# Kernel tuning notes

Measured on AMD Instinct MI355X. Metric: run time of the kernel, lower is better.

Reference implementation:

```python
import jax, jax.numpy as jnp
import numpy as np

N_NODES = 50000


def gcn_conv(x, W, b, row, col, n):
    """PyG GCNConv with default add_self_loops=True, normalize=True.
    out[i] = sum_{e: col[e]=i} d^-1/2[row[e]] d^-1/2[i] * (x@W)[row[e]]
             + d^-1[i]*(x@W)[i] + b,  where d = in-degree + 1 (self-loop).
    """
    x_lin = x @ W                                   # [n, out_ch]
    ones = jnp.ones(row.shape[0], dtype=x.dtype)
    deg = jax.ops.segment_sum(ones, col, num_segments=n) + 1.0  # self-loop
    dinv = jax.lax.rsqrt(deg)                       # deg >= 1, safe
    norm = dinv[row] * dinv[col]                    # [E]
    msg = norm[:, None] * x_lin[row]                # [E, out_ch]
    agg = jax.ops.segment_sum(msg, col, num_segments=n)
    self_term = (dinv * dinv)[:, None] * x_lin      # self-loop contribution
    return agg + self_term + b


def setup_inputs() -> dict:
    key = jax.random.key(0)
    ks = jax.random.split(key, 10)
    in_ch, hid, out_ch = 128, 256, 64
    E = 800000
    x = jax.random.normal(ks[0], (N_NODES, in_ch), dtype=jnp.float32)
    edge_attr = jax.random.normal(ks[1], (E, 8), dtype=jnp.float32)  # unused by forward
    edge_index = jax.random.randint(ks[2], (2, E), 0, N_NODES, dtype=jnp.int64)
    def glorot(k, fan_in, fan_out):
        s = float(np.sqrt(6.0 / (fan_in + fan_out)))
        return jax.random.uniform(k, (fan_in, fan_out), jnp.float32, -s, s)
    return {
        "x": x,
        "edge_attr": edge_attr,
        "edge_index": edge_index,
        "W1": glorot(ks[3], in_ch, hid), "b1": jnp.zeros((hid,), jnp.float32),
        "W2": glorot(ks[4], hid, hid),  "b2": jnp.zeros((hid,), jnp.float32),
        "W3": glorot(ks[5], hid, out_ch), "b3": jnp.zeros((out_ch,), jnp.float32),
    }


def reference(x, edge_attr, edge_index, W1, b1, W2, b2, W3, b3):
    n = x.shape[0]
    row, col = edge_index[0], edge_index[1]
    h = jax.nn.sigmoid(gcn_conv(x, W1, b1, row, col, n))
    h = jax.nn.sigmoid(gcn_conv(h, W2, b2, row, col, n))
    # dropout(p=0.1) in eval mode is identity
    return gcn_conv(h, W3, b3, row, col, n)
```

## Files before the change

### kernel.cpp

```cpp
#include <hip/hip_runtime.h>
#include <hip/hip_bf16.h>

typedef __bf16 bf16x8_t __attribute__((ext_vector_type(8)));
typedef float f32x4_t __attribute__((ext_vector_type(4)));
typedef float f32x2_t __attribute__((ext_vector_type(2)));

__device__ __forceinline__ float bits2f(unsigned int u) {
    union { unsigned int u; float f; } c; c.u = u; return c.f;
}
__device__ __forceinline__ unsigned short f2bf_bits(float f) {
    __hip_bfloat16 h = __float2bfloat16(f);
    return __builtin_bit_cast(unsigned short, h);
}
__device__ __forceinline__ f32x2_t unpack_bf2(unsigned int u) {
    return (f32x2_t){bits2f(u << 16), bits2f(u & 0xffff0000u)};
}

__global__ void sentinel_fill(float* __restrict__ out, int n) {
    int i = blockIdx.x * blockDim.x + threadIdx.x;
    if (i < n) out[i] = 100.0f;
}

__global__ void detect_ei(const unsigned int* __restrict__ ei, int* __restrict__ flags) {
    int lane = threadIdx.x;
    int cz = 0;
    #pragma unroll
    for (int j = 0; j < 4; ++j) {
        int idx = lane * 4 + j;
        cz += (ei[2 * idx + 1] == 0u);
    }
    #pragma unroll
    for (int off = 32; off; off >>= 1) cz += __shfl_down(cz, off);
    if (lane == 0) flags[0] = (cz > 200);
}


__global__ void count_rank_dual2(const int* __restrict__ ei, int* __restrict__ cnt,
                                 int* __restrict__ rank, int* __restrict__ c32,
                                 int* __restrict__ r32, int E, int M,
                                 const int* __restrict__ flags) {
    int e = blockIdx.x * blockDim.x + threadIdx.x;
    if (e < E) {
        int r, c;
        if (flags[0]) { r = ei[2 * e]; c = ei[2 * E + 2 * e]; }
        else          { r = ei[e];     c = ei[E + e]; }
        c32[e] = c;
        r32[e] = r;
        int rk = 0;
        if ((unsigned)c < (unsigned)M) rk = atomicAdd(&cnt[c], 1);
        rank[e] = rk;
    }
}

__global__ void scan_blocks(const int* __restrict__ cnt, int* __restrict__ excl,
                            int* __restrict__ bsum, int n) {
    int tid = threadIdx.x;
    int i = blockIdx.x * 256 + tid;
    int lane = tid & 63, wv = tid >> 6;
    __shared__ int ws[4];
    int v = (i < n) ? cnt[i] : 0;
    int s = v;
    #pragma unroll
    for (int off = 1; off < 64; off <<= 1) {
        int t = __shfl_up(s, off);
        if (lane >= off) s += t;
    }
    if (lane == 63) ws[wv] = s;
    __syncthreads();
    if (tid == 0) { int a = 0; for (int q = 0; q < 4; ++q) { int t = ws[q]; ws[q] = a; a += t; } }
    __syncthreads();
    int ex = s - v + ws[wv];
    if (i < n) excl[i] = ex;
    if (tid == 255) bsum[blockIdx.x] = ex + v;
}

__global__ void scan_bsums(const int* __restrict__ bsum, int* __restrict__ boff,
                           int nb, int* __restrict__ colptr, int n) {
    int tid = threadIdx.x, lane = tid & 63, wv = tid >> 6;
    __shared__ int ws[4];
    __shared__ int carry;
    if (tid == 0) carry = 0;
    __syncthreads();
    for (int base = 0; base < nb; base += 256) {
        int i = base + tid;
        int v = (i < nb) ? bsum[i] : 0;
        int s = v;
        #pragma unroll
        for (int off = 1; off < 64; off <<= 1) {
            int t = __shfl_up(s, off);
            if (lane >= off) s += t;
        }
        if (lane == 63) ws[wv] = s;
        __syncthreads();
        if (tid == 0) { int a = carry; for (int q = 0; q < 4; ++q) { int t = ws[q]; ws[q] = a; a += t; } carry = a; }
        __syncthreads();
        int ex = s - v + ws[wv];
        if (i < nb) boff[i] = ex;
        __syncthreads();
    }
    if (tid == 0) colptr[n] = carry;
}

__global__ void scan_add_dinv(const int* __restrict__ excl, const int* __restrict__ boff,
                              const int* __restrict__ cnt, int* __restrict__ colptr,
                              float* __restrict__ dinv, int n) {
    int i = blockIdx.x * 256 + threadIdx.x;
    if (i < n) {
        colptr[i] = excl[i] + boff[blockIdx.x];
        dinv[i] = rsqrtf((float)cnt[i] + 1.0f);
    }
}

__global__ void fill_csr_part2(const int* __restrict__ c32, const int* __restrict__ r32,
                               const int* __restrict__ colptr, const int* __restrict__ rank,
                               int* __restrict__ esrc, int E, int M, int psz) {
    int part = blockIdx.x & 7;
    int e = (blockIdx.x >> 3) * 256 + threadIdx.x;
    int lo = part * psz;
    int hi = lo + psz; if (hi > M) hi = M;
    if (e < E) {
        int c = c32[e];
        if (c >= lo && c < hi) {
            int r = r32[e];
            if ((unsigned)r < (unsigned)M) {
                int p = colptr[c] + rank[e];
                if ((unsigned)p < (unsigned)E) esrc[p] = r;
            }
        }
    }
}

__global__ void prep_fused(const float* __restrict__ x, const float* __restrict__ dinv,
                           unsigned char* __restrict__ xs8,
                           const float* __restrict__ W1, const float* __restrict__ W2,
                           const float* __restrict__ W3,
                           unsigned short* __restrict__ Wt1, unsigned short* __restrict__ Wt2,
                           unsigned short* __restrict__ Wt3,
                           int M, int nps) {
    if ((int)blockIdx.x < nps) {
        int i = blockIdx.x * 256 + threadIdx.x;
        if (i < M * 32) {
            int row = i >> 5;
            float dv = dinv[row];
            float4 v = *(const float4*)(x + (size_t)i * 4);
            unsigned u = __builtin_amdgcn_cvt_pk_fp8_f32(v.x * dv, v.y * dv, 0, false);
            u = __builtin_amdgcn_cvt_pk_fp8_f32(v.z * dv, v.w * dv, u, true);
            *(unsigned*)(xs8 + (size_t)i * 4) = u;
        }
    } else {
        int i = ((int)blockIdx.x - nps) * 256 + threadIdx.x;
        if (i < 32768) {
            int k = i >> 8, n = i & 255;
            Wt1[n * 128 + k] = f2bf_bits(W1[i]);
        } else if (i < 32768 + 65536) {
            int j = i - 32768;
            int k = j >> 8, n = j & 255;
            Wt2[n * 256 + k] = f2bf_bits(W2[j]);
        } else if (i < 114688) {
            int j = i - 98304;
            int k = j >> 6, n = j & 63;
            Wt3[n * 256 + k] = f2bf_bits(W3[j]);
        }
    }
}

template<int K, int BN, int NTOT, int EPI>
__global__ __launch_bounds__(256) void gemm_tile(
    const __bf16* __restrict__ A,
    const unsigned short* __restrict__ Bt,
    const float* __restrict__ dinv,
    const float* __restrict__ bias,
    void* __restrict__ Y,
    int M)
{
    constexpr int KS = (K > 128) ? 128 : K;
    constexpr int KP = KS + 8;
    constexpr int NT = BN / 2 / 16;
    __shared__ unsigned short Bs[BN * KP];

    const int tid  = threadIdx.x;
    const int lane = tid & 63;
    const int wave = tid >> 6;
    const int wm   = wave >> 1;
    const int wn   = wave & 1;
    const int quad = lane >> 4;
    const int l16  = lane & 15;
    const int n0   = blockIdx.y * BN;

    int mrow[4];
#pragma unroll
    for (int mt = 0; mt < 4; ++mt) {
        int r = blockIdx.x * 128 + wm * 64 + mt * 16 + l16;
        mrow[mt] = (r < M) ? r : (M - 1);
    }

    f32x4_t acc[4][NT];
#pragma unroll
    for (int mt = 0; mt < 4; ++mt)
#pragma unroll
        for (int t = 0; t < NT; ++t) acc[mt][t] = (f32x4_t){0.f, 0.f, 0.f, 0.f};

    const unsigned short* BsW = &Bs[(wn * (BN / 2)) * KP];

    for (int kh = 0; kh < K; kh += KS) {
        constexpr int CH = BN * KS / 8;
        for (int idx = tid; idx < CH; idx += 256) {
            int n  = idx / (KS / 8);
            int k8 = idx - n * (KS / 8);
            uint4 v = *(const uint4*)(Bt + (size_t)(n0 + n) * K + kh + k8 * 8);
            *(uint4*)&Bs[n * KP + k8 * 8] = v;
        }
        __syncthreads();

#pragma unroll
        for (int kc = 0; kc < KS; kc += 32) {
            bf16x8_t a[4], b[NT];
#pragma unroll
            for (int mt = 0; mt < 4; ++mt)
                a[mt] = *(const bf16x8_t*)(A + (size_t)mrow[mt] * K + kh + kc + quad * 8);
#pragma unroll
            for (int t = 0; t < NT; ++t)
                b[t] = *(const bf16x8_t*)&BsW[(t * 16 + l16) * KP + kc + quad * 8];
#pragma unroll
            for (int mt = 0; mt < 4; ++mt)
#pragma unroll
                for (int t = 0; t < NT; ++t)
                    acc[mt][t] = __builtin_amdgcn_mfma_f32_16x16x32_bf16(a[mt], b[t], acc[mt][t], 0, 0, 0);
        }
        if (kh + KS < K) __syncthreads();
    }

    float bv[NT];
    if constexpr (EPI == 1) {
#pragma unroll
        for (int t = 0; t < NT; ++t)
            bv[t] = bias[n0 + wn * (BN / 2) + t * 16 + l16];
    }

#pragma unroll
    for (int mt = 0; mt < 4; ++mt) {
        int rowbase = blockIdx.x * 128 + wm * 64 + mt * 16 + quad * 4;
#pragma unroll
        for (int r = 0; r < 4; ++r) {
            int rrow = rowbase + r;
            if (rrow < M) {
                if constexpr (EPI == 0) {
                    float dv = dinv[rrow];
#pragma unroll
                    for (int t = 0; t < NT; ++t) {
                        int ccol = n0 + wn * (BN / 2) + t * 16 + l16;
                        ((__hip_bfloat16*)Y)[(size_t)rrow * NTOT + ccol] =
                            __float2bfloat16(acc[mt][t][r] * dv);
                    }
                } else if constexpr (EPI == 1) {
#pragma unroll
                    for (int t = 0; t < NT; ++t) {
                        int ccol = n0 + wn * (BN / 2) + t * 16 + l16;
                        float o = acc[mt][t][r] + bv[t];
                        o = 1.f / (1.f + __expf(-o));
                        ((__hip_bfloat16*)Y)[(size_t)rrow * NTOT + ccol] = __float2bfloat16(o);
                    }
                } else {
                    float dv = dinv[rrow];
#pragma unroll
                    for (int t = 0; t < NT; ++t) {
                        int ccol = n0 + wn * (BN / 2) + t * 16 + l16;
                        float o = acc[mt][t][r] * dv;
                        int pk = __builtin_amdgcn_cvt_pk_fp8_f32(o, o, 0, false);
                        ((unsigned char*)Y)[(size_t)rrow * NTOT + ccol] = (unsigned char)(pk & 0xff);
                    }
                }
            }
        }
    }
}

__global__ __launch_bounds__(256) void aggregate_fp8_v4(
    const unsigned char* __restrict__ Y8,
    const int* __restrict__ colptr,
    const int* __restrict__ esrc,
    const float* __restrict__ dinv,
    const float* __restrict__ bias,
    unsigned short* __restrict__ H,
    int M, int Etot)
{
    const int lane = threadIdx.x & 63;
    const int wave = threadIdx.x >> 6;
    int node = blockIdx.x * 4 + wave;
    if (node >= M) return;

    int s = colptr[node];
    int e = colptr[node + 1];
    if (s < 0) s = 0;
    if (e > Etot) e = Etot;
    if (e < s) e = s;
    int n = e - s;

    const char* Yb = (const char*)Y8;
    const unsigned lb = (unsigned)(lane * 4);

    unsigned su = *(const unsigned*)(Yb + (((unsigned)node) << 8) + lb);

    f32x2_t a0 = {0.f, 0.f}, a1 = {0.f, 0.f};

    auto gather8 = [&](unsigned* u, int base) {
        #pragma unroll
        for (int k = 0; k < 8; ++k) {
            unsigned off = (((unsigned)esrc[s + base + k]) << 8) + lb;
            u[k] = *(const unsigned*)(Yb + off);
        }
    };
    auto acc8 = [&](const unsigned* u) {
        #pragma unroll
        for (int k = 0; k < 8; ++k) {
            a0 += __builtin_amdgcn_cvt_pk_f32_fp8(u[k], false);
            a1 += __builtin_amdgcn_cvt_pk_f32_fp8(u[k], true);
        }
    };

    unsigned ua[8], ub[8];
    int NB = n >> 3;
    if (NB > 0) {
        gather8(ua, 0);
        int i = 1;
        for (; i + 1 < NB; i += 2) {
            gather8(ub, i << 3);
            acc8(ua);
            gather8(ua, (i + 1) << 3);
            acc8(ub);
        }
        if (i < NB) {
            gather8(ub, i << 3);
            acc8(ua);
            acc8(ub);
        } else {
            acc8(ua);
        }
    }
    #pragma unroll 2
    for (int t = NB << 3; t < n; ++t) {
        unsigned off = (((unsigned)esrc[s + t]) << 8) + lb;
        unsigned u = *(const unsigned*)(Yb + off);
        a0 += __builtin_amdgcn_cvt_pk_f32_fp8(u, false);
        a1 += __builtin_amdgcn_cvt_pk_f32_fp8(u, true);
    }
    a0 += __builtin_amdgcn_cvt_pk_f32_fp8(su, false);
    a1 += __builtin_amdgcn_cvt_pk_f32_fp8(su, true);

    float dv = dinv[node];
    float4 bv = *(const float4*)(bias + lane * 4);
    float o0 = a0[0] * dv + bv.x;
    float o1 = a0[1] * dv + bv.y;
    float o2 = a1[0] * dv + bv.z;
    float o3 = a1[1] * dv + bv.w;
    o0 = 1.f / (1.f + __expf(-o0));
    o1 = 1.f / (1.f + __expf(-o1));
    o2 = 1.f / (1.f + __expf(-o2));
    o3 = 1.f / (1.f + __expf(-o3));
    uint2 st;
    st.x = (unsigned)f2bf_bits(o0) | ((unsigned)f2bf_bits(o1) << 16);
    st.y = (unsigned)f2bf_bits(o2) | ((unsigned)f2bf_bits(o3) << 16);
    *(uint2*)(H + (size_t)node * 256 + lane * 4) = st;
}

__global__ __launch_bounds__(256) void aggregate_xs8(
    const unsigned char* __restrict__ X8,
    const int* __restrict__ colptr,
    const int* __restrict__ esrc,
    const float* __restrict__ dinv,
    unsigned short* __restrict__ xa,
    int M, int Etot)
{
    const int lane = threadIdx.x & 63;
    const int wave = threadIdx.x >> 6;
    const int l5 = lane & 31;
    const int g  = lane >> 5;
    int node = blockIdx.x * 4 + wave;
    if (node >= M) return;

    int s = colptr[node];
    int e = colptr[node + 1];
    if (s < 0) s = 0;
    if (e > Etot) e = Etot;
    if (e < s) e = s;
    int n = e - s;

    const char* Yb = (const char*)X8;
    const unsigned lb = (unsigned)(l5 * 4);

    unsigned su = 0;
    if (g == 0) su = *(const unsigned*)(Yb + (((unsigned)node) << 7) + lb);

    f32x2_t a0 = {0.f, 0.f}, a1 = {0.f, 0.f};

    auto gather4 = [&](unsigned* u, int base) {
        #pragma unroll
        for (int k = 0; k < 4; ++k) {
            unsigned off = (((unsigned)esrc[s + base + 2 * k + g]) << 7) + lb;
            u[k] = *(const unsigned*)(Yb + off);
        }
    };
    auto acc4 = [&](const unsigned* u) {
        #pragma unroll
        for (int k = 0; k < 4; ++k) {
            a0 += __builtin_amdgcn_cvt_pk_f32_fp8(u[k], false);
            a1 += __builtin_amdgcn_cvt_pk_f32_fp8(u[k], true);
        }
    };

    unsigned ua[4], ub[4];
    int NB = n >> 3;
    if (NB > 0) {
        gather4(ua, 0);
        int i = 1;
        for (; i + 1 < NB; i += 2) {
            gather4(ub, i << 3);
            acc4(ua);
            gather4(ua, (i + 1) << 3);
            acc4(ub);
        }
        if (i < NB) {
            gather4(ub, i << 3);
            acc4(ua);
            acc4(ub);
        } else {
            acc4(ua);
        }
    }
    for (int t = NB << 3; t + g < n; t += 2) {
        unsigned off = (((unsigned)esrc[s + t + g]) << 7) + lb;
        unsigned u = *(const unsigned*)(Yb + off);
        a0 += __builtin_amdgcn_cvt_pk_f32_fp8(u, false);
        a1 += __builtin_amdgcn_cvt_pk_f32_fp8(u, true);
    }
    if (g == 0) {
        a0 += __builtin_amdgcn_cvt_pk_f32_fp8(su, false);
        a1 += __builtin_amdgcn_cvt_pk_f32_fp8(su, true);
    }

    a0[0] += __shfl_xor(a0[0], 32);
    a0[1] += __shfl_xor(a0[1], 32);
    a1[0] += __shfl_xor(a1[0], 32);
    a1[1] += __shfl_xor(a1[1], 32);

    if (g == 0) {
        float dv = dinv[node];
        uint2 st;
        st.x = (unsigned)f2bf_bits(a0[0] * dv) | ((unsigned)f2bf_bits(a0[1] * dv) << 16);
        st.y = (unsigned)f2bf_bits(a1[0] * dv) | ((unsigned)f2bf_bits(a1[1] * dv) << 16);
        *(uint2*)(xa + (size_t)node * 128 + l5 * 4) = st;
    }
}

__global__ __launch_bounds__(256) void aggregate_bf16_64_v4(
    const unsigned short* __restrict__ Yin,
    const int* __restrict__ colptr,
    const int* __restrict__ esrc,
    const float* __restrict__ dinv,
    const float* __restrict__ bias,
    float* __restrict__ out,
    int M, int Etot)
{
    const int lane = threadIdx.x & 63;
    const int wave = threadIdx.x >> 6;
    const int l5 = lane & 31;
    const int g  = lane >> 5;
    int node = blockIdx.x * 4 + wave;
    if (node >= M) return;

    int s = colptr[node];
    int e = colptr[node + 1];
    if (s < 0) s = 0;
    if (e > Etot) e = Etot;
    if (e < s) e = s;
    int n = e - s;

    const char* Yb = (const char*)Yin;
    const unsigned lb = (unsigned)(l5 * 4);

    unsigned su = 0;
    if (g == 0) su = *(const unsigned*)(Yb + (((unsigned)node) << 7) + lb);

    f32x2_t a = {0.f, 0.f};

    auto gather4 = [&](unsigned* u, int base) {
        #pragma unroll
        for (int k = 0; k < 4; ++k) {
            unsigned off = (((unsigned)esrc[s + base + 2 * k + g]) << 7) + lb;
            u[k] = *(const unsigned*)(Yb + off);
        }
    };
    auto acc4 = [&](const unsigned* u) {
        #pragma unroll
        for (int k = 0; k < 4; ++k) a += unpack_bf2(u[k]);
    };

    unsigned ua[4], ub[4];
    int NB = n >> 3;
    if (NB > 0) {
        gather4(ua, 0);
        int i = 1;
        for (; i + 1 < NB; i += 2) {
            gather4(ub, i << 3);
            acc4(ua);
            gather4(ua, (i + 1) << 3);
            acc4(ub);
        }
        if (i < NB) {
            gather4(ub, i << 3);
            acc4(ua);
            acc4(ub);
        } else {
            acc4(ua);
        }
    }
    for (int t = NB << 3; t + g < n; t += 2) {
        unsigned off = (((unsigned)esrc[s + t + g]) << 7) + lb;
        unsigned u = *(const unsigned*)(Yb + off);
        a += unpack_bf2(u);
    }
    if (g == 0) a += unpack_bf2(su);

    a[0] += __shfl_xor(a[0], 32);
    a[1] += __shfl_xor(a[1], 32);

    if (g == 0) {
        float dv = dinv[node];
        float2 bv = *(const float2*)(bias + l5 * 2);
        float2 st;
        st.x = a[0] * dv + bv.x;
        st.y = a[1] * dv + bv.y;
        *(float2*)(out + (size_t)node * 64 + l5 * 2) = st;
    }
}


extern "C" void kernel_launch(void* const* d_in, const int* in_sizes, int n_in,
                              void* d_out, int out_size, void* d_ws, size_t ws_size,
                              hipStream_t stream)
{
    int iEI = 2, iW1 = 3, iB1 = 4, iW2 = 5, iB2 = 6, iW3 = 7, iB3 = 8;
    if (n_in == 8) { iEI = 1; iW1 = 2; iB1 = 3; iW2 = 4; iB2 = 5; iW3 = 6; iB3 = 7; }

    const float* x  = (const float*)d_in[0];
    const int* ei   = (const int*)d_in[iEI];
    const float* W1 = (const float*)d_in[iW1];
    const float* b1 = (const float*)d_in[iB1];
    const float* W2 = (const float*)d_in[iW2];
    const float* b2 = (const float*)d_in[iB2];
    const float* W3 = (const float*)d_in[iW3];
    const float* b3 = (const float*)d_in[iB3];

    const int M = in_sizes[0] / 128;
    const int E = in_sizes[iEI] / 2;
    const int NB = (M + 255) / 256;
    const int PSZ = (M + 7) / 8;

    auto rnd = [](size_t b) { return (b + 255) & ~(size_t)255; };
    size_t needed = rnd(64 * 4)
                  + rnd((size_t)M * 4) * 2
                  + rnd((size_t)(M + 1) * 4)
                  + rnd((size_t)M * 4)
                  + rnd((size_t)(NB + 1) * 4) * 2
                  + rnd((size_t)E * 4) * 4
                  + rnd((size_t)256 * 128 * 2)
                  + rnd((size_t)256 * 256 * 2)
                  + rnd((size_t)64 * 256 * 2)
                  + rnd((size_t)M * 256 * 2) * 2;
    if (ws_size < needed) {
        sentinel_fill<<<(out_size + 255) / 256, 256, 0, stream>>>((float*)d_out, out_size);
        return;
    }

    char* p = (char*)d_ws;
    auto alloc = [&](size_t bytes) {
        char* r = p;
        p += (bytes + 255) & ~(size_t)255;
        return r;
    };
    int* flags  = (int*)alloc(64 * 4);
    float* dinv = (float*)alloc((size_t)M * 4);
    int* cnt    = (int*)alloc((size_t)M * 4);
    int* colptr = (int*)alloc((size_t)(M + 1) * 4);
    int* excl   = (int*)alloc((size_t)M * 4);
    int* bsum   = (int*)alloc((size_t)(NB + 1) * 4);
    int* boff   = (int*)alloc((size_t)(NB + 1) * 4);
    int* esrc   = (int*)alloc((size_t)E * 4);
    int* rank   = (int*)alloc((size_t)E * 4);
    int* c32    = (int*)alloc((size_t)E * 4);
    int* r32    = (int*)alloc((size_t)E * 4);
    unsigned short* Wt1 = (unsigned short*)alloc((size_t)256 * 128 * 2);
    unsigned short* Wt2 = (unsigned short*)alloc((size_t)256 * 256 * 2);
    unsigned short* Wt3 = (unsigned short*)alloc((size_t)64 * 256 * 2);
    __hip_bfloat16* ybuf = (__hip_bfloat16*)alloc((size_t)M * 256 * 2);
    __hip_bfloat16* hbuf = (__hip_bfloat16*)alloc((size_t)M * 256 * 2);

    unsigned char* xs8 = (unsigned char*)ybuf;
    unsigned short* xa = (unsigned short*)ybuf + (size_t)M * 128;
    unsigned char*  y8 = (unsigned char*)ybuf;

    detect_ei<<<1, 64, 0, stream>>>((const unsigned int*)ei, flags);

    hipMemsetAsync(cnt, 0, (size_t)M * 4, stream);
    count_rank_dual2<<<(E + 255) / 256, 256, 0, stream>>>(ei, cnt, rank, c32, r32, E, M, flags);
    scan_blocks<<<NB, 256, 0, stream>>>(cnt, excl, bsum, M);
    scan_bsums<<<1, 256, 0, stream>>>(bsum, boff, NB, colptr, M);
    scan_add_dinv<<<NB, 256, 0, stream>>>(excl, boff, cnt, colptr, dinv, M);
    fill_csr_part2<<<((E + 255) / 256) * 8, 256, 0, stream>>>(
        c32, r32, colptr, rank, esrc, E, M, PSZ);

    int gmb = (M + 127) / 128;
    int ga  = (M + 3) / 4;
    int nps = (M * 32 + 255) / 256;

    prep_fused<<<nps + 448, 256, 0, stream>>>(
        x, dinv, xs8, W1, W2, W3, Wt1, Wt2, Wt3, M, nps);

    aggregate_xs8<<<ga, 256, 0, stream>>>(
        xs8, colptr, esrc, dinv, xa, M, E);
    gemm_tile<128, 128, 256, 1><<<dim3(gmb, 2), 256, 0, stream>>>(
        (const __bf16*)xa, Wt1, dinv, b1, hbuf, M);
    gemm_tile<256, 128, 256, 2><<<dim3(gmb, 2), 256, 0, stream>>>(
        (const __bf16*)hbuf, Wt2, dinv, b2, y8, M);
    aggregate_fp8_v4<<<ga, 256, 0, stream>>>(
        y8, colptr, esrc, dinv, b2, (unsigned short*)hbuf, M, E);
    gemm_tile<256, 64, 64, 0><<<dim3(gmb, 1), 256, 0, stream>>>(
        (const __bf16*)hbuf, Wt3, dinv, b3, ybuf, M);
    aggregate_bf16_64_v4<<<ga, 256, 0, stream>>>(
        (const unsigned short*)ybuf, colptr, esrc, dinv, b3, (float*)d_out, M, E);
}
```

Baseline: 329.6 us.

## Split fp8 layer-2 features into 128-column chunks and aggregate each chunk separately

The layer-2 GEMM epilogue now writes the fp8 output in two column-chunk planes of 128 bytes per row instead of 256-byte rows. The aggregation kernel is rewritten so each block handles one chunk for a group of nodes. Each wave splits its edges between two half-waves that each gather 128-byte rows, and the partial sums are combined with a cross-lane shuffle. The aim is to shrink the working set per chunk so gathered rows fit better in L2 and to interleave the chunk blocks of neighbouring node groups, at the cost of reading colptr/esrc twice and doing an extra reduction.

```diff
diff --git a/kernel.cpp b/kernel.cpp
--- a/kernel.cpp
+++ b/kernel.cpp
@@ -267,7 +267,9 @@
                         int ccol = n0 + wn * (BN / 2) + t * 16 + l16;
                         float o = acc[mt][t][r] * dv;
                         int pk = __builtin_amdgcn_cvt_pk_fp8_f32(o, o, 0, false);
-                        ((unsigned char*)Y)[(size_t)rrow * NTOT + ccol] = (unsigned char)(pk & 0xff);
+                        size_t choff = (size_t)(ccol >> 7) * ((size_t)M * 128)
+                                     + (size_t)rrow * 128 + (ccol & 127);
+                        ((unsigned char*)Y)[choff] = (unsigned char)(pk & 0xff);
                     }
                 }
             }
@@ -275,18 +277,25 @@
     }
 }
 
-__global__ __launch_bounds__(256) void aggregate_fp8_v4(
-    const unsigned char* __restrict__ Y8,
+__global__ __launch_bounds__(256) void aggregate_fp8_x2(
+    const unsigned char* __restrict__ Y8c,
     const int* __restrict__ colptr,
     const int* __restrict__ esrc,
     const float* __restrict__ dinv,
     const float* __restrict__ bias,
     unsigned short* __restrict__ H,
-    int M, int Etot)
+    int M, int Etot, int ga)
 {
     const int lane = threadIdx.x & 63;
     const int wave = threadIdx.x >> 6;
-    int node = blockIdx.x * 4 + wave;
+    const int l5 = lane & 31;
+    const int g2 = lane >> 5;
+
+    int s8 = blockIdx.x & 7;
+    int chunk = s8 >> 2;
+    int grp = (blockIdx.x >> 3) * 4 + (s8 & 3);
+    if (grp >= ga) return;
+    int node = grp * 4 + wave;
     if (node >= M) return;
 
     int s = colptr[node];
@@ -296,71 +305,81 @@
     if (e < s) e = s;
     int n = e - s;
 
-    const char* Yb = (const char*)Y8;
-    const unsigned lb = (unsigned)(lane * 4);
-
-    unsigned su = *(const unsigned*)(Yb + (((unsigned)node) << 8) + lb);
+    const char* Yb = (const char*)(Y8c + (size_t)chunk * ((size_t)M * 128));
+    const unsigned lb = (unsigned)(l5 * 4);
+
+    unsigned su = 0;
+    if (g2 == 0) su = *(const unsigned*)(Yb + ((unsigned)node) * 128u + lb);
 
     f32x2_t a0 = {0.f, 0.f}, a1 = {0.f, 0.f};
 
-    auto gather8 = [&](unsigned* u, int base) {
+    auto gather4 = [&](unsigned* u, int base) {
         #pragma unroll
-        for (int k = 0; k < 8; ++k) {
-            unsigned off = (((unsigned)esrc[s + base + k]) << 8) + lb;
+        for (int k = 0; k < 4; ++k) {
+            unsigned off = (((unsigned)esrc[s + base + 2 * k + g2]) * 128u) + lb;
             u[k] = *(const unsigned*)(Yb + off);
         }
     };
-    auto acc8 = [&](const unsigned* u) {
+    auto acc4 = [&](const unsigned* u) {
         #pragma unroll
-        for (int k = 0; k < 8; ++k) {
+        for (int k = 0; k < 4; ++k) {
             a0 += __builtin_amdgcn_cvt_pk_f32_fp8(u[k], false);
             a1 += __builtin_amdgcn_cvt_pk_f32_fp8(u[k], true);
         }
     };
 
-    unsigned ua[8], ub[8];
+    unsigned ua[4], ub[4];
     int NB = n >> 3;
     if (NB > 0) {
-        gather8(ua, 0);
+        gather4(ua, 0);
         int i = 1;
         for (; i + 1 < NB; i += 2) {
-            gather8(ub, i << 3);
-            acc8(ua);
-            gather8(ua, (i + 1) << 3);
-            acc8(ub);
+            gather4(ub, i << 3);
+            acc4(ua);
+            gather4(ua, (i + 1) << 3);
+            acc4(ub);
         }
         if (i < NB) {
-            gather8(ub, i << 3);
-            acc8(ua);
-            acc8(ub);
+            gather4(ub, i << 3);
+            acc4(ua);
+            acc4(ub);
         } else {
-            acc8(ua);
-        }
-    }
-    #pragma unroll 2
-    for (int t = NB << 3; t < n; ++t) {
-        unsigned off = (((unsigned)esrc[s + t]) << 8) + lb;
+            acc4(ua);
+        }
+    }
+    for (int t = NB << 3; t + g2 < n; t += 2) {
+        unsigned off = (((unsigned)esrc[s + t + g2]) * 128u) + lb;
         unsigned u = *(const unsigned*)(Yb + off);
         a0 += __builtin_amdgcn_cvt_pk_f32_fp8(u, false);
         a1 += __builtin_amdgcn_cvt_pk_f32_fp8(u, true);
     }
-    a0 += __builtin_amdgcn_cvt_pk_f32_fp8(su, false);
-    a1 += __builtin_amdgcn_cvt_pk_f32_fp8(su, true);
-
-    float dv = dinv[node];
-    float4 bv = *(const float4*)(bias + lane * 4);
-    float o0 = a0[0] * dv + bv.x;
-    float o1 = a0[1] * dv + bv.y;
-    float o2 = a1[0] * dv + bv.z;
-    float o3 = a1[1] * dv + bv.w;
-    o0 = 1.f / (1.f + __expf(-o0));
-    o1 = 1.f / (1.f + __expf(-o1));
-    o2 = 1.f / (1.f + __expf(-o2));
-    o3 = 1.f / (1.f + __expf(-o3));
-    uint2 st;
-    st.x = (unsigned)f2bf_bits(o0) | ((unsigned)f2bf_bits(o1) << 16);
-    st.y = (unsigned)f2bf_bits(o2) | ((unsigned)f2bf_bits(o3) << 16);
-    *(uint2*)(H + (size_t)node * 256 + lane * 4) = st;
+    if (g2 == 0) {
+        a0 += __builtin_amdgcn_cvt_pk_f32_fp8(su, false);
+        a1 += __builtin_amdgcn_cvt_pk_f32_fp8(su, true);
+    }
+
+    a0[0] += __shfl_xor(a0[0], 32);
+    a0[1] += __shfl_xor(a0[1], 32);
+    a1[0] += __shfl_xor(a1[0], 32);
+    a1[1] += __shfl_xor(a1[1], 32);
+
+    if (g2 == 0) {
+        float dv = dinv[node];
+        int chb = chunk * 128 + l5 * 4;
+        float4 bv = *(const float4*)(bias + chb);
+        float o0 = a0[0] * dv + bv.x;
+        float o1 = a0[1] * dv + bv.y;
+        float o2 = a1[0] * dv + bv.z;
+        float o3 = a1[1] * dv + bv.w;
+        o0 = 1.f / (1.f + __expf(-o0));
+        o1 = 1.f / (1.f + __expf(-o1));
+        o2 = 1.f / (1.f + __expf(-o2));
+        o3 = 1.f / (1.f + __expf(-o3));
+        uint2 st;
+        st.x = (unsigned)f2bf_bits(o0) | ((unsigned)f2bf_bits(o1) << 16);
+        st.y = (unsigned)f2bf_bits(o2) | ((unsigned)f2bf_bits(o3) << 16);
+        *(uint2*)(H + (size_t)node * 256 + chb) = st;
+    }
 }
 
 __global__ __launch_bounds__(256) void aggregate_xs8(
@@ -612,6 +631,7 @@
     int gmb = (M + 127) / 128;
     int ga  = (M + 3) / 4;
     int nps = (M * 32 + 255) / 256;
+    int nsup = (ga + 3) / 4;
 
     prep_fused<<<nps + 448, 256, 0, stream>>>(
         x, dinv, xs8, W1, W2, W3, Wt1, Wt2, Wt3, M, nps);
@@ -622,8 +642,8 @@
         (const __bf16*)xa, Wt1, dinv, b1, hbuf, M);
     gemm_tile<256, 128, 256, 2><<<dim3(gmb, 2), 256, 0, stream>>>(
         (const __bf16*)hbuf, Wt2, dinv, b2, y8, M);
-    aggregate_fp8_v4<<<ga, 256, 0, stream>>>(
-        y8, colptr, esrc, dinv, b2, (unsigned short*)hbuf, M, E);
+    aggregate_fp8_x2<<<nsup * 8, 256, 0, stream>>>(
+        y8, colptr, esrc, dinv, b2, (unsigned short*)hbuf, M, E, ga);
     gemm_tile<256, 64, 64, 0><<<dim3(gmb, 1), 256, 0, stream>>>(
         (const __bf16*)hbuf, Wt3, dinv, b3, ybuf, M);
     aggregate_bf16_64_v4<<<ga, 256, 0, stream>>>(
```

New measurement: 342.9 us. +4.0%, slower.
